# Performance work log

Hardware: AMD Instinct MI355X
Metric: run time of the kernel (lower is better)

The kernel has to match this reference:

```python
import jax, jax.numpy as jnp
import numpy as np

B, CH, H, W, D = 2, 32, 256, 512, 192


def setup_inputs() -> dict:
    key = jax.random.key(0)
    ks = jax.random.split(key, 10)
    def w(k, shape, fan_in):
        return jax.random.normal(k, shape, jnp.float32) * (1.0 / np.sqrt(fan_in))
    return {
        "x": jax.random.normal(ks[0], (B, CH, H, W), jnp.float32),
        "y": jax.random.normal(ks[1], (B, CH, H, W), jnp.float32),
        # encoder: 1x1 convs ch->64->32->1 (shared for x and y)
        "w1": w(ks[2], (64, CH), CH), "b1": w(ks[3], (64,), CH),
        "w2": w(ks[4], (32, 64), 64), "b2": w(ks[5], (32,), 64),
        "w3": w(ks[6], (1, 32), 32), "b3": w(ks[7], (1,), 32),
        # decoderl: 1x1 conv maxdisp->maxdisp (original code applies decoderl to BOTH volumes)
        "wd": w(ks[8], (D, D), D), "bd": w(ks[9], (D,), D),
    }


def _conv1x1(w, b, h):  # [O,C] x [B,C,H,W] -> [B,O,H,W]
    return jnp.einsum("oc,bchw->bohw", w, h) + b[None, :, None, None]


def _encoder(x, w1, b1, w2, b2, w3, b3):
    h = jax.nn.relu(x)
    h = jax.nn.relu(_conv1x1(w1, b1, h))
    h = jax.nn.relu(_conv1x1(w2, b2, h))
    h = jax.nn.relu(_conv1x1(w3, b3, h))
    return h[:, 0]  # squeeze channel -> [B,H,W]


def _cost_volumes(xf, yf):
    # costx[b,d,h,w] = xf[b,h,w+d] * yf[b,h,w]   (0 where w+d >= W)
    # costy[b,d,h,w] = xf[b,h,w]   * yf[b,h,w-d] (0 where w-d < 0)
    dgrid = jnp.arange(D)
    wgrid = jnp.arange(W)
    x_pad = jnp.pad(xf, ((0, 0), (0, 0), (0, D)))          # zero pad right
    xg = x_pad[:, :, wgrid[None, :] + dgrid[:, None]]       # [B,H,D,W]
    costx = (xg * yf[:, :, None, :]).transpose(0, 2, 1, 3)  # [B,D,H,W]
    y_pad = jnp.pad(yf, ((0, 0), (0, 0), (D, 0)))           # zero pad left
    yg = y_pad[:, :, wgrid[None, :] - dgrid[:, None] + D]   # [B,H,D,W]
    costy = (xf[:, :, None, :] * yg).transpose(0, 2, 1, 3)  # [B,D,H,W]
    return costx, costy


def reference(x, y, w1, b1, w2, b2, w3, b3, wd, bd):
    xf = _encoder(x, w1, b1, w2, b2, w3, b3)
    yf = _encoder(y, w1, b1, w2, b2, w3, b3)
    costx, costy = _cost_volumes(xf, yf)
    probx = jax.nn.softmax(_conv1x1(wd, bd, costx), axis=1)
    proby = jax.nn.softmax(_conv1x1(wd, bd, costy), axis=1)  # decoderl used for both, as in source
    disp_vals = jnp.arange(D, dtype=probx.dtype)
    dispx = jnp.einsum("bdhw,d->bhw", probx, disp_vals)
    dispy = jnp.einsum("bdhw,d->bhw", proby, disp_vals)
    return dispx, dispy
```

## Files before the change

kernel.cpp:

```cpp
#include <hip/hip_runtime.h>


typedef __attribute__((ext_vector_type(8))) __bf16 bf16x8;
typedef __attribute__((ext_vector_type(4))) float  f32x4;

#define MFMA16x16x32(a,b,c) __builtin_amdgcn_mfma_f32_16x16x32_bf16((a),(b),(c),0,0,0)

constexpr int WW  = 512;
constexpr int HW  = 256 * 512;
constexpr int CHW = 32 * HW;
constexpr float LOG2E = 1.4426950408889634f;

constexpr size_t XFB_OFF = 0;
constexpr size_t WDP_OFF = 2 * 262144 * 2;
constexpr size_t BDP_OFF = WDP_OFF + 73728;

__global__ __launch_bounds__(512)
void panet_encode(const float* __restrict__ gx,  const float* __restrict__ gy,
                  const float* __restrict__ gw1, const float* __restrict__ gb1,
                  const float* __restrict__ gw2, const float* __restrict__ gb2,
                  const float* __restrict__ gw3, const float* __restrict__ gb3,
                  const float* __restrict__ gwd, const float* __restrict__ gbd,
                  char* __restrict__ ws)
{
  const int blk = blockIdx.x;
  const int tid = threadIdx.x;

  if (blk >= 1024) {
    const int pi = blk - 1024;
    unsigned short* wdp = (unsigned short*)(ws + WDP_OFF);
    for (int idx = tid; idx < 12 * 192; idx += 512) {
      const int oo = idx / 192;
      const int k  = idx - oo * 192;
      const int o  = 12 * pi + oo;
      const int half = (o >= 96) ? 1 : 0;
      const int op = o - 96 * half;
      const __bf16 v = (__bf16)gwd[o * 192 + k];
      const int byt = half * 36864 + op * 384 + ((2 * k) ^ ((op & 7) << 4));
      wdp[byt >> 1] = __builtin_bit_cast(unsigned short, v);
    }
    if (pi == 0) {
      float* bdp = (float*)(ws + BDP_OFF);
      if (tid < 192) bdp[tid] = gbd[tid] * LOG2E;
    }
    return;
  }

  const int t    = blk >> 9;
  const int bh   = blk & 511;
  const int lane = tid & 63;
  const int m    = lane & 15;
  const int g    = lane >> 4;
  const int wid  = tid >> 6;

  bf16x8 A1[4], A2[2][2];
  f32x4  bias1[4], bias2[2], w3v[2];
  #pragma unroll
  for (int Mt = 0; Mt < 4; ++Mt) {
    const float* p = gw1 + (16 * Mt + m) * 32 + 4 * g;
    const f32x4 u0 = *(const f32x4*)p;
    const f32x4 u1 = *(const f32x4*)(p + 16);
    #pragma unroll
    for (int j = 0; j < 4; ++j) { A1[Mt][j] = (__bf16)u0[j]; A1[Mt][j + 4] = (__bf16)u1[j]; }
    bias1[Mt] = *(const f32x4*)(gb1 + 16 * Mt + 4 * g);
  }
  #pragma unroll
  for (int Mt = 0; Mt < 2; ++Mt) {
    #pragma unroll
    for (int s = 0; s < 2; ++s) {
      const float* p = gw2 + (16 * Mt + m) * 64 + 32 * s + 4 * g;
      const f32x4 u0 = *(const f32x4*)p;
      const f32x4 u1 = *(const f32x4*)(p + 16);
      #pragma unroll
      for (int j = 0; j < 4; ++j) { A2[Mt][s][j] = (__bf16)u0[j]; A2[Mt][s][j + 4] = (__bf16)u1[j]; }
    }
    bias2[Mt] = *(const f32x4*)(gb2 + 16 * Mt + 4 * g);
    w3v[Mt]   = *(const f32x4*)(gw3 + 16 * Mt + 4 * g);
  }
  const float b3s = gb3[0];
  const f32x4 zf4 = {0.f, 0.f, 0.f, 0.f};
  const float* base = (t ? gy : gx) + (bh >> 8) * CHW + (bh & 255) * WW;
  unsigned short* xfb = (unsigned short*)(ws + XFB_OFF) + t * 262144 + bh * 512;

  for (int u = wid; u < 32; u += 8) {
    const int w0 = u << 4;
    const float* src = base + w0 + m;

    bf16x8 B1;
    #pragma unroll
    for (int j = 0; j < 8; ++j) {
      const int c = 16 * (j >> 2) + 4 * g + (j & 3);
      B1[j] = (__bf16)fmaxf(src[c * HW], 0.f);
    }
    f32x4 acc1[4];
    #pragma unroll
    for (int Mt = 0; Mt < 4; ++Mt) acc1[Mt] = MFMA16x16x32(A1[Mt], B1, zf4);

    bf16x8 B2[2];
    #pragma unroll
    for (int s = 0; s < 2; ++s) {
      #pragma unroll
      for (int j = 0; j < 4; ++j) {
        B2[s][j]     = (__bf16)fmaxf(acc1[2 * s][j]     + bias1[2 * s][j],     0.f);
        B2[s][j + 4] = (__bf16)fmaxf(acc1[2 * s + 1][j] + bias1[2 * s + 1][j], 0.f);
      }
    }
    f32x4 acc2[2];
    #pragma unroll
    for (int Mt = 0; Mt < 2; ++Mt)
      acc2[Mt] = MFMA16x16x32(A2[Mt][1], B2[1], MFMA16x16x32(A2[Mt][0], B2[0], zf4));

    float s3 = 0.f;
    #pragma unroll
    for (int Mt = 0; Mt < 2; ++Mt)
      #pragma unroll
      for (int r = 0; r < 4; ++r)
        s3 += w3v[Mt][r] * fmaxf(acc2[Mt][r] + bias2[Mt][r], 0.f);
    s3 += __shfl_xor(s3, 16);
    s3 += __shfl_xor(s3, 32);
    const float val = fmaxf(s3 + b3s, 0.f);

    if (lane < 16)
      xfb[w0 + m] = __builtin_bit_cast(unsigned short, (__bf16)val);
  }
}

constexpr int CPS    = 1424;
constexpr int K2_WD  = 0;
constexpr int K2_HK  = 36864;
constexpr int K2_BD  = K2_HK + 11392;
constexpr int K2_LDS = K2_BD + 768;

__global__ __launch_bounds__(512)
void panet_corr(const char* __restrict__ ws, float* __restrict__ gout)
{
  __shared__ __align__(16) char lds[K2_LDS];
  const int blk  = blockIdx.x;
  const int dir  = blk >> 9;
  const int bh   = blk & 511;
  const int tid  = threadIdx.x;
  const int lane = tid & 63;
  const int m    = lane & 15;
  const int g    = lane >> 4;
  const int wid  = tid >> 6;

  const unsigned short* xfb = (const unsigned short*)(ws + XFB_OFF);
  const unsigned short* hs = xfb + (dir ? 262144 : 0) + bh * 512;
  const unsigned short* ss = xfb + (dir ? 0 : 262144) + bh * 512;

  {
    const f32x4* src = (const f32x4*)(ws + WDP_OFF);
    f32x4* dst = (f32x4*)(lds + K2_WD);
    for (int i = tid; i < 36864 / 16; i += 512) dst[i] = src[i];
    int* zp = (int*)(lds + K2_HK);
    for (int i = tid; i < 11392 / 4; i += 512) zp[i] = 0;
    const float* bdp = (const float*)(ws + BDP_OFF);
    if (tid < 192) ((float*)(lds + K2_BD))[tid] = bdp[tid];
  }
  __syncthreads();
  #pragma unroll
  for (int c = 0; c < 8; ++c) {
    const int e = tid;
    if (e + c <= 511) {
      ((unsigned short*)(lds + K2_HK + c * CPS))[e] = hs[dir ? (511 - e - c) : (e + c)];
    }
  }
  __syncthreads();

  const int Xm   = (m & 7) << 4;
  const int arow = m * 384;
  const float g4 = 4.0f * (float)g;
  float stM[2][2], stS[2][2], stW[2][2];

  for (int half = 0; half < 2; ++half) {
    if (half) {
      __syncthreads();
      const f32x4* src = (const f32x4*)(ws + WDP_OFF + 36864);
      f32x4* dst = (f32x4*)(lds + K2_WD);
      for (int i = tid; i < 36864 / 16; i += 512) dst[i] = src[i];
      __syncthreads();
    }
    for (int ch = 0; ch < 2; ++ch) {
      int laneB[2]; float sc[2];
      #pragma unroll
      for (int nt = 0; nt < 2; ++nt) {
        const int col = wid * 64 + ch * 32 + nt * 16 + m;
        const int I0  = dir ? (511 - col) : col;
        const int c   = I0 & 7;
        laneB[nt] = c * CPS + 2 * (I0 - c) + 16 * g;
        sc[nt] = LOG2E * __builtin_bit_cast(float, (unsigned)ss[col] << 16);
      }
      bf16x8 bfr[6][2];
      #pragma unroll
      for (int ks = 0; ks < 6; ++ks) {
        bfr[ks][0] = *(const bf16x8*)(lds + K2_HK + laneB[0] + (ks << 6));
        bfr[ks][1] = *(const bf16x8*)(lds + K2_HK + laneB[1] + (ks << 6));
      }

      float mx0 = -3.4e38f, mx1 = -3.4e38f;
      float s0 = 0.f, s1 = 0.f, ws0 = 0.f, ws1 = 0.f;

      #pragma unroll 1
      for (int mp = 0; mp < 3; ++mp) {
        f32x4 a00 = {0,0,0,0}, a01 = {0,0,0,0}, a10 = {0,0,0,0}, a11 = {0,0,0,0};
        #pragma unroll
        for (int ks = 0; ks < 6; ++ks) {
          const int inner = ((ks << 6) + (g << 4)) ^ Xm;
          const char* ap = lds + K2_WD + (mp * 2) * 6144 + arow + inner;
          const bf16x8 af0 = *(const bf16x8*)(ap);
          const bf16x8 af1 = *(const bf16x8*)(ap + 6144);
          a00 = MFMA16x16x32(af0, bfr[ks][0], a00);
          a01 = MFMA16x16x32(af0, bfr[ks][1], a01);
          a10 = MFMA16x16x32(af1, bfr[ks][0], a10);
          a11 = MFMA16x16x32(af1, bfr[ks][1], a11);
        }
        const int tbase = 6 * half + 2 * mp;
        const f32x4 bd0 = *(const f32x4*)(lds + K2_BD + tbase * 64 + 16 * g);
        const f32x4 bd1 = *(const f32x4*)(lds + K2_BD + (tbase + 1) * 64 + 16 * g);
        const float ob = (float)(96 * half + 32 * mp);

        {
          f32x4 L0, L1;
          #pragma unroll
          for (int r = 0; r < 4; ++r) {
            L0[r] = fmaf(sc[0], a00[r], bd0[r]);
            L1[r] = fmaf(sc[0], a10[r], bd1[r]);
          }
          const float pm = fmaxf(fmaxf(fmaxf(L0[0], L0[1]), fmaxf(L0[2], L0[3])),
                                 fmaxf(fmaxf(L1[0], L1[1]), fmaxf(L1[2], L1[3])));
          const float nm = fmaxf(mx0, pm);
          const float f  = exp2f(mx0 - nm);
          float ls = 0.f, lw = 0.f;
          #pragma unroll
          for (int r = 0; r < 4; ++r) {
            const float p0 = exp2f(L0[r] - nm);
            const float p1 = exp2f(L1[r] - nm);
            ls += p0 + p1;
            lw += (ob + (float)r) * p0 + (ob + 16.f + (float)r) * p1;
          }
          s0 = fmaf(s0, f, ls);  ws0 = fmaf(ws0, f, lw);  mx0 = nm;
        }
        {
          f32x4 L0, L1;
          #pragma unroll
          for (int r = 0; r < 4; ++r) {
            L0[r] = fmaf(sc[1], a01[r], bd0[r]);
            L1[r] = fmaf(sc[1], a11[r], bd1[r]);
          }
          const float pm = fmaxf(fmaxf(fmaxf(L0[0], L0[1]), fmaxf(L0[2], L0[3])),
                                 fmaxf(fmaxf(L1[0], L1[1]), fmaxf(L1[2], L1[3])));
          const float nm = fmaxf(mx1, pm);
          const float f  = exp2f(mx1 - nm);
          float ls = 0.f, lw = 0.f;
          #pragma unroll
          for (int r = 0; r < 4; ++r) {
            const float p0 = exp2f(L0[r] - nm);
            const float p1 = exp2f(L1[r] - nm);
            ls += p0 + p1;
            lw += (ob + (float)r) * p0 + (ob + 16.f + (float)r) * p1;
          }
          s1 = fmaf(s1, f, ls);  ws1 = fmaf(ws1, f, lw);  mx1 = nm;
        }
      }

      #pragma unroll
      for (int nt = 0; nt < 2; ++nt) {
        const float mx = nt ? mx1 : mx0;
        const float s  = nt ? s1  : s0;
        const float w  = nt ? ws1 : ws0;
        float M = fmaxf(mx, __shfl_xor(mx, 16));
        M = fmaxf(M, __shfl_xor(M, 32));
        const float f = exp2f(mx - M);
        float sr = s * f;
        float wr = (w + g4 * s) * f;
        sr += __shfl_xor(sr, 16); sr += __shfl_xor(sr, 32);
        wr += __shfl_xor(wr, 16); wr += __shfl_xor(wr, 32);
        if (half == 0) {
          stM[ch][nt] = M;  stS[ch][nt] = sr;  stW[ch][nt] = wr;
        } else {
          const float MM = fmaxf(stM[ch][nt], M);
          const float f0 = exp2f(stM[ch][nt] - MM);
          const float f1 = exp2f(M - MM);
          stS[ch][nt] = stS[ch][nt] * f0 + sr * f1;
          stW[ch][nt] = stW[ch][nt] * f0 + wr * f1;
          stM[ch][nt] = MM;
        }
      }
    }
  }

  float* outp = gout + dir * 262144 + bh * 512;
  #pragma unroll
  for (int ch = 0; ch < 2; ++ch)
    #pragma unroll
    for (int nt = 0; nt < 2; ++nt)
      if (lane < 16)
        outp[wid * 64 + ch * 32 + nt * 16 + m] = stW[ch][nt] / stS[ch][nt];
}

extern "C" void kernel_launch(void* const* d_in, const int* in_sizes, int n_in,
                              void* d_out, int out_size, void* d_ws, size_t ws_size,
                              hipStream_t stream) {
  const float* x  = (const float*)d_in[0];
  const float* y  = (const float*)d_in[1];
  const float* w1 = (const float*)d_in[2];
  const float* b1 = (const float*)d_in[3];
  const float* w2 = (const float*)d_in[4];
  const float* b2 = (const float*)d_in[5];
  const float* w3 = (const float*)d_in[6];
  const float* b3 = (const float*)d_in[7];
  const float* wd = (const float*)d_in[8];
  const float* bd = (const float*)d_in[9];
  char* ws = (char*)d_ws;

  panet_encode<<<1040, 512, 0, stream>>>(x, y, w1, b1, w2, b2, w3, b3, wd, bd, ws);
  panet_corr<<<1024, 512, 0, stream>>>(ws, (float*)d_out);
}
```

Measured before the change: 94.46 us.

## Switch correlation decoder to 32x32x16 MFMA with three-stage padded weight staging

The decoder GEMM in the correlation kernel now uses 32x32x16 bf16 MFMAs instead of 16x16x32. The 192x192 weight matrix is staged into LDS in three 64-row chunks with a padded 400-byte row stride, replacing the XOR-swizzled two-half layout. The online softmax now runs over 32 outputs per lane with a single cross-half shuffle reduction at the end. This cuts LDS A-fragment reads and cross-lane reductions per output, at the cost of an extra sync stage, more accumulator registers (four 16-wide accumulators), and possibly fewer waves resident per CU.

```diff
diff --git a/kernel.cpp b/kernel.cpp
--- a/kernel.cpp
+++ b/kernel.cpp
@@ -1,10 +1,12 @@
 #include <hip/hip_runtime.h>
 
 
-typedef __attribute__((ext_vector_type(8))) __bf16 bf16x8;
-typedef __attribute__((ext_vector_type(4))) float  f32x4;
-
-#define MFMA16x16x32(a,b,c) __builtin_amdgcn_mfma_f32_16x16x32_bf16((a),(b),(c),0,0,0)
+typedef __attribute__((ext_vector_type(8)))  __bf16 bf16x8;
+typedef __attribute__((ext_vector_type(4)))  float  f32x4;
+typedef __attribute__((ext_vector_type(16))) float  f32x16;
+
+#define MFMA32(a,b,c) __builtin_amdgcn_mfma_f32_32x32x16_bf16((a),(b),(c),0,0,0)
+#define MFMA16(a,b,c) __builtin_amdgcn_mfma_f32_16x16x32_bf16((a),(b),(c),0,0,0)
 
 constexpr int WW  = 512;
 constexpr int HW  = 256 * 512;
@@ -33,11 +35,8 @@
       const int oo = idx / 192;
       const int k  = idx - oo * 192;
       const int o  = 12 * pi + oo;
-      const int half = (o >= 96) ? 1 : 0;
-      const int op = o - 96 * half;
       const __bf16 v = (__bf16)gwd[o * 192 + k];
-      const int byt = half * 36864 + op * 384 + ((2 * k) ^ ((op & 7) << 4));
-      wdp[byt >> 1] = __builtin_bit_cast(unsigned short, v);
+      wdp[o * 192 + k] = __builtin_bit_cast(unsigned short, v);
     }
     if (pi == 0) {
       float* bdp = (float*)(ws + BDP_OFF);
@@ -94,7 +93,7 @@
     }
     f32x4 acc1[4];
     #pragma unroll
-    for (int Mt = 0; Mt < 4; ++Mt) acc1[Mt] = MFMA16x16x32(A1[Mt], B1, zf4);
+    for (int Mt = 0; Mt < 4; ++Mt) acc1[Mt] = MFMA16(A1[Mt], B1, zf4);
 
     bf16x8 B2[2];
     #pragma unroll
@@ -108,7 +107,7 @@
     f32x4 acc2[2];
     #pragma unroll
     for (int Mt = 0; Mt < 2; ++Mt)
-      acc2[Mt] = MFMA16x16x32(A2[Mt][1], B2[1], MFMA16x16x32(A2[Mt][0], B2[0], zf4));
+      acc2[Mt] = MFMA16(A2[Mt][1], B2[1], MFMA16(A2[Mt][0], B2[0], zf4));
 
     float s3 = 0.f;
     #pragma unroll
@@ -127,7 +126,7 @@
 
 constexpr int CPS    = 1424;
 constexpr int K2_WD  = 0;
-constexpr int K2_HK  = 36864;
+constexpr int K2_HK  = 25600;
 constexpr int K2_BD  = K2_HK + 11392;
 constexpr int K2_LDS = K2_BD + 768;
 
@@ -140,8 +139,8 @@
   const int bh   = blk & 511;
   const int tid  = threadIdx.x;
   const int lane = tid & 63;
-  const int m    = lane & 15;
-  const int g    = lane >> 4;
+  const int l31  = lane & 31;
+  const int h    = lane >> 5;
   const int wid  = tid >> 6;
 
   const unsigned short* xfb = (const unsigned short*)(ws + XFB_OFF);
@@ -149,9 +148,6 @@
   const unsigned short* ss = xfb + (dir ? 0 : 262144) + bh * 512;
 
   {
-    const f32x4* src = (const f32x4*)(ws + WDP_OFF);
-    f32x4* dst = (f32x4*)(lds + K2_WD);
-    for (int i = tid; i < 36864 / 16; i += 512) dst[i] = src[i];
     int* zp = (int*)(lds + K2_HK);
     for (int i = tid; i < 11392 / 4; i += 512) zp[i] = 0;
     const float* bdp = (const float*)(ws + BDP_OFF);
@@ -161,141 +157,96 @@
   #pragma unroll
   for (int c = 0; c < 8; ++c) {
     const int e = tid;
-    if (e + c <= 511) {
+    if (e + c <= 511)
       ((unsigned short*)(lds + K2_HK + c * CPS))[e] = hs[dir ? (511 - e - c) : (e + c)];
-    }
-  }
-  __syncthreads();
-
-  const int Xm   = (m & 7) << 4;
-  const int arow = m * 384;
-  const float g4 = 4.0f * (float)g;
-  float stM[2][2], stS[2][2], stW[2][2];
-
-  for (int half = 0; half < 2; ++half) {
-    if (half) {
-      __syncthreads();
-      const f32x4* src = (const f32x4*)(ws + WDP_OFF + 36864);
-      f32x4* dst = (f32x4*)(lds + K2_WD);
-      for (int i = tid; i < 36864 / 16; i += 512) dst[i] = src[i];
-      __syncthreads();
-    }
-    for (int ch = 0; ch < 2; ++ch) {
-      int laneB[2]; float sc[2];
-      #pragma unroll
-      for (int nt = 0; nt < 2; ++nt) {
-        const int col = wid * 64 + ch * 32 + nt * 16 + m;
-        const int I0  = dir ? (511 - col) : col;
-        const int c   = I0 & 7;
-        laneB[nt] = c * CPS + 2 * (I0 - c) + 16 * g;
-        sc[nt] = LOG2E * __builtin_bit_cast(float, (unsigned)ss[col] << 16);
-      }
-      bf16x8 bfr[6][2];
-      #pragma unroll
-      for (int ks = 0; ks < 6; ++ks) {
-        bfr[ks][0] = *(const bf16x8*)(lds + K2_HK + laneB[0] + (ks << 6));
-        bfr[ks][1] = *(const bf16x8*)(lds + K2_HK + laneB[1] + (ks << 6));
-      }
-
-      float mx0 = -3.4e38f, mx1 = -3.4e38f;
-      float s0 = 0.f, s1 = 0.f, ws0 = 0.f, ws1 = 0.f;
-
-      #pragma unroll 1
-      for (int mp = 0; mp < 3; ++mp) {
-        f32x4 a00 = {0,0,0,0}, a01 = {0,0,0,0}, a10 = {0,0,0,0}, a11 = {0,0,0,0};
+  }
+
+  int bfb[2]; float sc[2];
+  #pragma unroll
+  for (int ct = 0; ct < 2; ++ct) {
+    const int col = wid * 64 + ct * 32 + l31;
+    const int I0  = dir ? (511 - col) : col;
+    const int cc  = I0 & 7;
+    bfb[ct] = K2_HK + cc * CPS + 2 * (I0 - cc) + 16 * h;
+    sc[ct]  = LOG2E * __builtin_bit_cast(float, (unsigned)ss[col] << 16);
+  }
+  const int baseA = l31 * 400 + 16 * h;
+
+  float stM[2] = {-3.4e38f, -3.4e38f};
+  float stS[2] = {0.f, 0.f};
+  float stW[2] = {0.f, 0.f};
+
+  for (int stage = 0; stage < 3; ++stage) {
+    if (stage) __syncthreads();
+    for (int i = tid; i < 1536; i += 512) {
+      const f32x4 v = *(const f32x4*)(ws + WDP_OFF + stage * 24576 + i * 16);
+      const int row = i / 24;
+      const int within = (i - row * 24) * 16;
+      *(f32x4*)(lds + K2_WD + row * 400 + within) = v;
+    }
+    __syncthreads();
+
+    f32x16 a00 = {0}, a01 = {0}, a10 = {0}, a11 = {0};
+    #pragma unroll 2
+    for (int ks = 0; ks < 12; ++ks) {
+      const int ko = 32 * ks;
+      const bf16x8 af0 = *(const bf16x8*)(lds + K2_WD + baseA + ko);
+      const bf16x8 af1 = *(const bf16x8*)(lds + K2_WD + baseA + 12800 + ko);
+      const bf16x8 bf0 = *(const bf16x8*)(lds + bfb[0] + ko);
+      const bf16x8 bf1 = *(const bf16x8*)(lds + bfb[1] + ko);
+      a00 = MFMA32(af0, bf0, a00);
+      a01 = MFMA32(af0, bf1, a01);
+      a10 = MFMA32(af1, bf0, a10);
+      a11 = MFMA32(af1, bf1, a11);
+    }
+
+    #pragma unroll
+    for (int ct = 0; ct < 2; ++ct) {
+      const f32x16 A0 = ct ? a01 : a00;
+      const f32x16 A1 = ct ? a11 : a10;
+      float L[32];
+      #pragma unroll
+      for (int q = 0; q < 4; ++q) {
+        const int rbase0 = 64 * stage + 8 * q + 4 * h;
+        const f32x4 bd0 = *(const f32x4*)(lds + K2_BD + rbase0 * 4);
+        const f32x4 bd1 = *(const f32x4*)(lds + K2_BD + (rbase0 + 32) * 4);
         #pragma unroll
-        for (int ks = 0; ks < 6; ++ks) {
-          const int inner = ((ks << 6) + (g << 4)) ^ Xm;
-          const char* ap = lds + K2_WD + (mp * 2) * 6144 + arow + inner;
-          const bf16x8 af0 = *(const bf16x8*)(ap);
-          const bf16x8 af1 = *(const bf16x8*)(ap + 6144);
-          a00 = MFMA16x16x32(af0, bfr[ks][0], a00);
-          a01 = MFMA16x16x32(af0, bfr[ks][1], a01);
-          a10 = MFMA16x16x32(af1, bfr[ks][0], a10);
-          a11 = MFMA16x16x32(af1, bfr[ks][1], a11);
-        }
-        const int tbase = 6 * half + 2 * mp;
-        const f32x4 bd0 = *(const f32x4*)(lds + K2_BD + tbase * 64 + 16 * g);
-        const f32x4 bd1 = *(const f32x4*)(lds + K2_BD + (tbase + 1) * 64 + 16 * g);
-        const float ob = (float)(96 * half + 32 * mp);
-
-        {
-          f32x4 L0, L1;
-          #pragma unroll
-          for (int r = 0; r < 4; ++r) {
-            L0[r] = fmaf(sc[0], a00[r], bd0[r]);
-            L1[r] = fmaf(sc[0], a10[r], bd1[r]);
-          }
-          const float pm = fmaxf(fmaxf(fmaxf(L0[0], L0[1]), fmaxf(L0[2], L0[3])),
-                                 fmaxf(fmaxf(L1[0], L1[1]), fmaxf(L1[2], L1[3])));
-          const float nm = fmaxf(mx0, pm);
-          const float f  = exp2f(mx0 - nm);
-          float ls = 0.f, lw = 0.f;
-          #pragma unroll
-          for (int r = 0; r < 4; ++r) {
-            const float p0 = exp2f(L0[r] - nm);
-            const float p1 = exp2f(L1[r] - nm);
-            ls += p0 + p1;
-            lw += (ob + (float)r) * p0 + (ob + 16.f + (float)r) * p1;
-          }
-          s0 = fmaf(s0, f, ls);  ws0 = fmaf(ws0, f, lw);  mx0 = nm;
-        }
-        {
-          f32x4 L0, L1;
-          #pragma unroll
-          for (int r = 0; r < 4; ++r) {
-            L0[r] = fmaf(sc[1], a01[r], bd0[r]);
-            L1[r] = fmaf(sc[1], a11[r], bd1[r]);
-          }
-          const float pm = fmaxf(fmaxf(fmaxf(L0[0], L0[1]), fmaxf(L0[2], L0[3])),
-                                 fmaxf(fmaxf(L1[0], L1[1]), fmaxf(L1[2], L1[3])));
-          const float nm = fmaxf(mx1, pm);
-          const float f  = exp2f(mx1 - nm);
-          float ls = 0.f, lw = 0.f;
-          #pragma unroll
-          for (int r = 0; r < 4; ++r) {
-            const float p0 = exp2f(L0[r] - nm);
-            const float p1 = exp2f(L1[r] - nm);
-            ls += p0 + p1;
-            lw += (ob + (float)r) * p0 + (ob + 16.f + (float)r) * p1;
-          }
-          s1 = fmaf(s1, f, ls);  ws1 = fmaf(ws1, f, lw);  mx1 = nm;
+        for (int r = 0; r < 4; ++r) {
+          L[4 * q + r]      = fmaf(sc[ct], A0[4 * q + r], bd0[r]);
+          L[16 + 4 * q + r] = fmaf(sc[ct], A1[4 * q + r], bd1[r]);
         }
       }
-
-      #pragma unroll
-      for (int nt = 0; nt < 2; ++nt) {
-        const float mx = nt ? mx1 : mx0;
-        const float s  = nt ? s1  : s0;
-        const float w  = nt ? ws1 : ws0;
-        float M = fmaxf(mx, __shfl_xor(mx, 16));
-        M = fmaxf(M, __shfl_xor(M, 32));
-        const float f = exp2f(mx - M);
-        float sr = s * f;
-        float wr = (w + g4 * s) * f;
-        sr += __shfl_xor(sr, 16); sr += __shfl_xor(sr, 32);
-        wr += __shfl_xor(wr, 16); wr += __shfl_xor(wr, 32);
-        if (half == 0) {
-          stM[ch][nt] = M;  stS[ch][nt] = sr;  stW[ch][nt] = wr;
-        } else {
-          const float MM = fmaxf(stM[ch][nt], M);
-          const float f0 = exp2f(stM[ch][nt] - MM);
-          const float f1 = exp2f(M - MM);
-          stS[ch][nt] = stS[ch][nt] * f0 + sr * f1;
-          stW[ch][nt] = stW[ch][nt] * f0 + wr * f1;
-          stM[ch][nt] = MM;
-        }
+      float pm = L[0];
+      #pragma unroll
+      for (int i = 1; i < 32; ++i) pm = fmaxf(pm, L[i]);
+      const float nm = fmaxf(stM[ct], pm);
+      const float f  = exp2f(stM[ct] - nm);
+      float ls = 0.f, lw = 0.f;
+      #pragma unroll
+      for (int i = 0; i < 32; ++i) {
+        const float p = exp2f(L[i] - nm);
+        const float o = (float)(64 * stage + ((i >> 4) << 5) + (i & 3) + (((i & 15) >> 2) << 3) + 4 * h);
+        ls += p;
+        lw = fmaf(o, p, lw);
       }
+      stS[ct] = fmaf(stS[ct], f, ls);
+      stW[ct] = fmaf(stW[ct], f, lw);
+      stM[ct] = nm;
     }
   }
 
   float* outp = gout + dir * 262144 + bh * 512;
   #pragma unroll
-  for (int ch = 0; ch < 2; ++ch)
-    #pragma unroll
-    for (int nt = 0; nt < 2; ++nt)
-      if (lane < 16)
-        outp[wid * 64 + ch * 32 + nt * 16 + m] = stW[ch][nt] / stS[ch][nt];
+  for (int ct = 0; ct < 2; ++ct) {
+    const float Mo = __shfl_xor(stM[ct], 32);
+    const float M  = fmaxf(stM[ct], Mo);
+    const float f  = exp2f(stM[ct] - M);
+    float sr = stS[ct] * f;
+    float wr = stW[ct] * f;
+    sr += __shfl_xor(sr, 32);
+    wr += __shfl_xor(wr, 32);
+    if (lane < 32) outp[wid * 64 + ct * 32 + l31] = wr / sr;
+  }
 }
 
 extern "C" void kernel_launch(void* const* d_in, const int* in_sizes, int n_in,
```

Result: faster. 89.24 us (-5.5%).
